# Kernel optimization log

Hardware: AMD Instinct MI355X
Metric: run time of the kernel (lower is better)

## Reference

```python
import jax, jax.numpy as jnp
import numpy as np

EPS = 1e-13

def dct_basis(n):
    # Orthonormal DCT-II basis: C[k, i] = s_k * cos(pi*(2i+1)*k / (2n))
    k = np.arange(n)[:, None]
    i = np.arange(n)[None, :]
    C = np.cos(np.pi * (2 * i + 1) * k / (2 * n))
    scale = np.full((n, 1), np.sqrt(2.0 / n))
    scale[0, 0] = np.sqrt(1.0 / n)
    return jnp.asarray(C * scale, dtype=jnp.float32)


def setup_inputs() -> dict:
    key = jax.random.key(0)
    B, C, H, W = 128, 3, 256, 256
    inputs = jax.random.normal(key, (B, C, H, W), dtype=jnp.float32)
    mean = jnp.asarray(-8.0, dtype=jnp.float32)
    std = jnp.asarray(6.0, dtype=jnp.float32)
    return {"inputs": inputs, "mean": mean, "std": std}


def reference(inputs, mean, std):
    H, W = inputs.shape[-2], inputs.shape[-1]
    CH = dct_basis(H)  # [H, H]
    CW = dct_basis(W)  # [W, W]
    # 2D DCT-II (ortho): out[..., k1, k2] = sum_ij CH[k1,i] * x[..., i, j] * CW[k2,j]
    x = jnp.einsum('hi,bcij,wj->bchw', CH, inputs, CW)
    x = jnp.log(jnp.abs(x) + EPS)
    return (x - mean) / std
```

## Files before the change

### kernel.cpp

```cpp
#include <hip/hip_runtime.h>
#include <cmath>


#define HN    256
#define NIMG  384

__global__ void basis_init(float* __restrict__ Tdf) {
    int idx = blockIdx.x * 256 + threadIdx.x;
    int i = idx >> 8, k = idx & 255;
    double c = cos(M_PI * (2.0 * i + 1.0) * (double)k / 512.0);
    double s = (k == 0) ? sqrt(1.0 / 256.0) : sqrt(2.0 / 256.0);
    Tdf[idx] = (float)(c * s);
}

__device__ __forceinline__ void decode_bx(int n, int& img, int& kg) {
    img = (n & 7) * 48 + (n >> 5);
    kg  = (n >> 3) & 3;
}

#define FMA16(S, V) \
    _Pragma("unroll") \
    for (int q = 0; q < 16; ++q) { \
        acc[q].x = fmaf(S[q], V.x, acc[q].x); \
        acc[q].y = fmaf(S[q], V.y, acc[q].y); \
        acc[q].z = fmaf(S[q], V.z, acc[q].z); \
        acc[q].w = fmaf(S[q], V.w, acc[q].w); \
    }

#define SLOAD16(D, P) \
    _Pragma("unroll") \
    for (int a = 0; a < 4; ++a) \
        *(float4*)&(D)[4 * a] = *(const float4*)((P) + 4 * a);

#define DCT_MAINLOOP(vp, sp) \
    float4 acc[16]; \
    _Pragma("unroll") \
    for (int q = 0; q < 16; ++q) acc[q] = make_float4(0.f, 0.f, 0.f, 0.f); \
    float4 xv0, xv1; float bs0[16], bs1[16]; \
    xv0 = *(const float4*)(vp); (vp) += HN; \
    xv1 = *(const float4*)(vp); (vp) += HN; \
    SLOAD16(bs0, sp); (sp) += HN; \
    SLOAD16(bs1, sp); (sp) += HN; \
    _Pragma("unroll 1") \
    for (int i = 0; i < HN - 2; i += 2) { \
        float4 xn0 = *(const float4*)(vp); (vp) += HN; \
        float sn0[16]; SLOAD16(sn0, sp); (sp) += HN; \
        FMA16(bs0, xv0); \
        xv0 = xn0; \
        _Pragma("unroll") \
        for (int q = 0; q < 16; ++q) bs0[q] = sn0[q]; \
        float4 xn1 = *(const float4*)(vp); (vp) += HN; \
        float sn1[16]; SLOAD16(sn1, sp); (sp) += HN; \
        FMA16(bs1, xv1); \
        xv1 = xn1; \
        _Pragma("unroll") \
        for (int q = 0; q < 16; ++q) bs1[q] = sn1[q]; \
    } \
    FMA16(bs0, xv0); \
    FMA16(bs1, xv1);

__global__ __launch_bounds__(256, 6) void t1_kernel(
    const float* __restrict__ X, const float* __restrict__ Tdf,
    float* __restrict__ T1t)
{
    int img, kg; decode_bx(blockIdx.x, img, kg);
    const int wave = threadIdx.x >> 6;
    const int lane = threadIdx.x & 63;
    const int k1b  = __builtin_amdgcn_readfirstlane(kg * 64 + wave * 16);

    const float* __restrict__ vp = X + (size_t)img * (HN * HN) + 4 * lane;
    const float* __restrict__ sp = Tdf + k1b;

    DCT_MAINLOOP(vp, sp)

    float* __restrict__ T1o =
        T1t + (size_t)img * (HN * HN) + (size_t)(4 * lane) * HN + k1b;
    const float* af = (const float*)acc;
    #pragma unroll
    for (int r = 0; r < 4; ++r)
        #pragma unroll
        for (int a = 0; a < 4; ++a) {
            float4 v = make_float4(af[4 * (4 * a + 0) + r],
                                   af[4 * (4 * a + 1) + r],
                                   af[4 * (4 * a + 2) + r],
                                   af[4 * (4 * a + 3) + r]);
            *(float4*)(T1o + r * HN + 4 * a) = v;
        }
}

__global__ __launch_bounds__(256, 6) void y_kernel(
    const float* __restrict__ T1t, const float* __restrict__ Tdf,
    const float* __restrict__ meanp, const float* __restrict__ stdp,
    float* __restrict__ out)
{
    int img, kg; decode_bx(blockIdx.x, img, kg);
    const int wave = threadIdx.x >> 6;
    const int lane = threadIdx.x & 63;
    const int k2b  = __builtin_amdgcn_readfirstlane(kg * 64 + wave * 16);

    const float* __restrict__ vp = T1t + (size_t)img * (HN * HN) + 4 * lane;
    const float* __restrict__ sp = Tdf + k2b;

    DCT_MAINLOOP(vp, sp)

    const float mean = meanp[0];
    const float stdv = stdp[0];
    float* __restrict__ O =
        out + (size_t)img * (HN * HN) + (size_t)(4 * lane) * HN + k2b;
    const float* af = (const float*)acc;
    #pragma unroll
    for (int r = 0; r < 4; ++r)
        #pragma unroll
        for (int a = 0; a < 4; ++a) {
            float4 v;
            v.x = (logf(fabsf(af[4 * (4 * a + 0) + r]) + 1e-13f) - mean) / stdv;
            v.y = (logf(fabsf(af[4 * (4 * a + 1) + r]) + 1e-13f) - mean) / stdv;
            v.z = (logf(fabsf(af[4 * (4 * a + 2) + r]) + 1e-13f) - mean) / stdv;
            v.w = (logf(fabsf(af[4 * (4 * a + 3) + r]) + 1e-13f) - mean) / stdv;
            *(float4*)(O + r * HN + 4 * a) = v;
        }
}

#define SLAB 32
__global__ __launch_bounds__(256, 3) void dct2_f32(
    const float* __restrict__ X, const float* __restrict__ Tdf,
    const float* __restrict__ meanp, const float* __restrict__ stdp,
    float* __restrict__ out)
{
    __shared__ union SU {
        struct { float Xs[8][HN]; float CHc[8][SLAB]; } p1;
        float Bc[16][HN];
    } u;
    __shared__ float T1s[SLAB][HN + 1];

    const int t   = threadIdx.x;
    const int img = blockIdx.x >> 3;
    const int k0  = (blockIdx.x & 7) * SLAB;
    const float* __restrict__ Xi = X + (size_t)img * (HN * HN);
    const int ci = t & 7;
    const int ib = t >> 3;

    float acc[8][4];
    #pragma unroll
    for (int q = 0; q < 8; ++q)
        #pragma unroll
        for (int r = 0; r < 4; ++r) acc[q][r] = 0.0f;

    for (int i0 = 0; i0 < HN; i0 += 8) {
        {
            int rr = t >> 5, cc = (t & 31) * 4;
            float4 a = *(const float4*)(Xi + (i0 + rr) * HN + cc);
            float4 b = *(const float4*)(Xi + (i0 + rr) * HN + cc + 128);
            *(float4*)&u.p1.Xs[rr][cc]       = a;
            *(float4*)&u.p1.Xs[rr][cc + 128] = b;
            u.p1.CHc[rr][t & 31] = Tdf[(i0 + rr) * HN + k0 + (t & 31)];
        }
        __syncthreads();
        #pragma unroll
        for (int ii = 0; ii < 8; ++ii) {
            float xr[8];
            *(float4*)&xr[0] = *(const float4*)&u.p1.Xs[ii][8 * ib];
            *(float4*)&xr[4] = *(const float4*)&u.p1.Xs[ii][8 * ib + 4];
            float ch[4];
            *(float4*)&ch[0] = *(const float4*)&u.p1.CHc[ii][4 * ci];
            #pragma unroll
            for (int q = 0; q < 8; ++q)
                #pragma unroll
                for (int r = 0; r < 4; ++r)
                    acc[q][r] = fmaf(ch[r], xr[q], acc[q][r]);
        }
        __syncthreads();
    }
    #pragma unroll
    for (int q = 0; q < 8; ++q)
        #pragma unroll
        for (int r = 0; r < 4; ++r)
            T1s[4 * ci + r][8 * ib + q] = acc[q][r];
    __syncthreads();

    float acc2[8][4];
    #pragma unroll
    for (int q = 0; q < 8; ++q)
        #pragma unroll
        for (int r = 0; r < 4; ++r) acc2[q][r] = 0.0f;

    for (int j0 = 0; j0 < HN; j0 += 16) {
        #pragma unroll
        for (int rep = 0; rep < 4; ++rep) {
            int idx = rep * 1024 + t * 4;
            int p = idx >> 8, c = idx & 255;
            *(float4*)&u.Bc[p][c] = *(const float4*)(Tdf + (j0 + p) * HN + c);
        }
        __syncthreads();
        #pragma unroll
        for (int p = 0; p < 16; ++p) {
            float a[4];
            #pragma unroll
            for (int r = 0; r < 4; ++r) a[r] = T1s[4 * ci + r][j0 + p];
            float b[8];
            *(float4*)&b[0] = *(const float4*)&u.Bc[p][8 * ib];
            *(float4*)&b[4] = *(const float4*)&u.Bc[p][8 * ib + 4];
            #pragma unroll
            for (int q = 0; q < 8; ++q)
                #pragma unroll
                for (int r = 0; r < 4; ++r)
                    acc2[q][r] = fmaf(a[r], b[q], acc2[q][r]);
        }
        __syncthreads();
    }

    const float mean = meanp[0];
    const float stdv = stdp[0];
    #pragma unroll
    for (int q = 0; q < 8; ++q)
        #pragma unroll
        for (int r = 0; r < 4; ++r) {
            float v = (logf(fabsf(acc2[q][r]) + 1e-13f) - mean) / stdv;
            T1s[4 * ci + r][8 * ib + q] = v;
        }
    __syncthreads();

    float* __restrict__ O = out + (size_t)img * (HN * HN) + (size_t)k0 * HN;
    #pragma unroll
    for (int rep = 0; rep < 8; ++rep) {
        int idx = rep * 1024 + t * 4;
        int row = idx >> 8, col = idx & 255;
        float4 v = make_float4(T1s[row][col], T1s[row][col + 1],
                               T1s[row][col + 2], T1s[row][col + 3]);
        *(float4*)(O + row * HN + col) = v;
    }
}

extern "C" void kernel_launch(void* const* d_in, const int* in_sizes, int n_in,
                              void* d_out, int out_size, void* d_ws, size_t ws_size,
                              hipStream_t stream) {
    const float* X     = (const float*)d_in[0];
    const float* meanp = (const float*)d_in[1];
    const float* stdp  = (const float*)d_in[2];

    float* Tdf = (float*)d_ws;
    const size_t T1_OFF    = 256 * 1024;
    const size_t T1_BYTES  = (size_t)NIMG * HN * HN * sizeof(float);

    basis_init<<<256, 256, 0, stream>>>(Tdf);

    if (ws_size >= T1_OFF + T1_BYTES) {
        float* T1 = (float*)((char*)d_ws + T1_OFF);
        t1_kernel<<<NIMG * 4, 256, 0, stream>>>(X, Tdf, T1);
        y_kernel <<<NIMG * 4, 256, 0, stream>>>(T1, Tdf, meanp, stdp,
                                                (float*)d_out);
    } else {
        dct2_f32<<<NIMG * 8, 256, 0, stream>>>(X, Tdf, meanp, stdp,
                                               (float*)d_out);
    }
}
```

Before: 442.9 us.

## Deepen main-loop software pipeline and lower launch-bounds occupancy hint

The FMA main loop becomes a four-stage prefetch pipeline: four input rows are held in flight while two basis rows are double-buffered and refilled in place after each FMA block. Launch bounds drop from 6 to 4 blocks per SM, giving the compiler more registers to keep these buffers live. The readfirstlane hint on the basis offset is also removed, so the compiler may no longer treat the basis loads as wave-uniform scalar loads. The intent is to hide more load latency per wave, at the cost of lower occupancy and a possible move of basis reads from scalar to vector memory.

```diff
diff --git a/kernel.cpp b/kernel.cpp
--- a/kernel.cpp
+++ b/kernel.cpp
@@ -21,57 +21,58 @@
 #define FMA16(S, V) \
     _Pragma("unroll") \
     for (int q = 0; q < 16; ++q) { \
-        acc[q].x = fmaf(S[q], V.x, acc[q].x); \
-        acc[q].y = fmaf(S[q], V.y, acc[q].y); \
-        acc[q].z = fmaf(S[q], V.z, acc[q].z); \
-        acc[q].w = fmaf(S[q], V.w, acc[q].w); \
-    }
-
-#define SLOAD16(D, P) \
+        acc[q].x = fmaf((S)[q], (V).x, acc[q].x); \
+        acc[q].y = fmaf((S)[q], (V).y, acc[q].y); \
+        acc[q].z = fmaf((S)[q], (V).z, acc[q].z); \
+        acc[q].w = fmaf((S)[q], (V).w, acc[q].w); \
+    }
+
+#define BLOAD(DST, P) \
     _Pragma("unroll") \
     for (int a = 0; a < 4; ++a) \
-        *(float4*)&(D)[4 * a] = *(const float4*)((P) + 4 * a);
-
-#define DCT_MAINLOOP(vp, sp) \
+        *(float4*)&(DST)[4 * a] = *(const float4*)((P) + 4 * a);
+
+#define DCT_PIPELINE(vp, bp) \
     float4 acc[16]; \
     _Pragma("unroll") \
     for (int q = 0; q < 16; ++q) acc[q] = make_float4(0.f, 0.f, 0.f, 0.f); \
-    float4 xv0, xv1; float bs0[16], bs1[16]; \
-    xv0 = *(const float4*)(vp); (vp) += HN; \
-    xv1 = *(const float4*)(vp); (vp) += HN; \
-    SLOAD16(bs0, sp); (sp) += HN; \
-    SLOAD16(bs1, sp); (sp) += HN; \
+    float4 vbuf[4]; \
+    float  bbuf[2][16]; \
+    _Pragma("unroll") \
+    for (int m = 0; m < 4; ++m) vbuf[m] = *(const float4*)((vp) + m * HN); \
+    BLOAD(bbuf[0], (bp) + 0 * HN); \
+    BLOAD(bbuf[1], (bp) + 1 * HN); \
     _Pragma("unroll 1") \
-    for (int i = 0; i < HN - 2; i += 2) { \
-        float4 xn0 = *(const float4*)(vp); (vp) += HN; \
-        float sn0[16]; SLOAD16(sn0, sp); (sp) += HN; \
-        FMA16(bs0, xv0); \
-        xv0 = xn0; \
+    for (int i = 0; i < HN - 4; i += 4) { \
         _Pragma("unroll") \
-        for (int q = 0; q < 16; ++q) bs0[q] = sn0[q]; \
-        float4 xn1 = *(const float4*)(vp); (vp) += HN; \
-        float sn1[16]; SLOAD16(sn1, sp); (sp) += HN; \
-        FMA16(bs1, xv1); \
-        xv1 = xn1; \
-        _Pragma("unroll") \
-        for (int q = 0; q < 16; ++q) bs1[q] = sn1[q]; \
+        for (int m = 0; m < 4; ++m) { \
+            FMA16(bbuf[m & 1], vbuf[m]); \
+            vbuf[m] = *(const float4*)((vp) + (m + 4) * HN); \
+            BLOAD(bbuf[m & 1], (bp) + (m + 2) * HN); \
+        } \
+        (vp) += 4 * HN; (bp) += 4 * HN; \
     } \
-    FMA16(bs0, xv0); \
-    FMA16(bs1, xv1);
-
-__global__ __launch_bounds__(256, 6) void t1_kernel(
+     \
+    FMA16(bbuf[0], vbuf[0]); \
+    BLOAD(bbuf[0], (bp) + 2 * HN);    \
+    FMA16(bbuf[1], vbuf[1]); \
+    BLOAD(bbuf[1], (bp) + 3 * HN);    \
+    FMA16(bbuf[0], vbuf[2]); \
+    FMA16(bbuf[1], vbuf[3]);
+
+__global__ __launch_bounds__(256, 4) void t1_kernel(
     const float* __restrict__ X, const float* __restrict__ Tdf,
     float* __restrict__ T1t)
 {
     int img, kg; decode_bx(blockIdx.x, img, kg);
     const int wave = threadIdx.x >> 6;
     const int lane = threadIdx.x & 63;
-    const int k1b  = __builtin_amdgcn_readfirstlane(kg * 64 + wave * 16);
+    const int k1b  = kg * 64 + wave * 16;
 
     const float* __restrict__ vp = X + (size_t)img * (HN * HN) + 4 * lane;
-    const float* __restrict__ sp = Tdf + k1b;
-
-    DCT_MAINLOOP(vp, sp)
+    const float* __restrict__ bp = Tdf + k1b;
+
+    DCT_PIPELINE(vp, bp)
 
     float* __restrict__ T1o =
         T1t + (size_t)img * (HN * HN) + (size_t)(4 * lane) * HN + k1b;
@@ -88,7 +89,7 @@
         }
 }
 
-__global__ __launch_bounds__(256, 6) void y_kernel(
+__global__ __launch_bounds__(256, 4) void y_kernel(
     const float* __restrict__ T1t, const float* __restrict__ Tdf,
     const float* __restrict__ meanp, const float* __restrict__ stdp,
     float* __restrict__ out)
@@ -96,12 +97,12 @@
     int img, kg; decode_bx(blockIdx.x, img, kg);
     const int wave = threadIdx.x >> 6;
     const int lane = threadIdx.x & 63;
-    const int k2b  = __builtin_amdgcn_readfirstlane(kg * 64 + wave * 16);
+    const int k2b  = kg * 64 + wave * 16;
 
     const float* __restrict__ vp = T1t + (size_t)img * (HN * HN) + 4 * lane;
-    const float* __restrict__ sp = Tdf + k2b;
-
-    DCT_MAINLOOP(vp, sp)
+    const float* __restrict__ bp = Tdf + k2b;
+
+    DCT_PIPELINE(vp, bp)
 
     const float mean = meanp[0];
     const float stdv = stdp[0];
```

After: 1.533 ms. +246.1%, slower.
